# Optimization experiments

Measured on AMD Instinct MI355X. Metric: run time of the kernel, lower is better.

## Reference

```python
import jax, jax.numpy as jnp
import numpy as np
from jax import lax

B, T, IN, H = 32, 512, 512, 512
NUM_LAYERS, NUM_DIR = 2, 2


def _lstm_layer(inputs, Wx, Wh, bx, bh, reverse):
    """inputs: [T,B,D]; Wx: [4H,D]; Wh: [4H,H]; bx,bh: [4H]. Returns (hs [T,B,H], hT, cT)."""
    Tn, Bn, _ = inputs.shape
    Hn = Wh.shape[1]
    # Precompute input-to-hidden projections for all timesteps (one big GEMM).
    xg = jnp.einsum('tbd,gd->tbg', inputs, Wx) + bx + bh  # [T,B,4H]
    if reverse:
        xg = xg[::-1]

    def step(carry, xg_t):
        h, c = carry
        g = xg_t + h @ Wh.T  # [B,4H]
        i, f, gg, o = jnp.split(g, 4, axis=-1)  # PyTorch LSTM gate order i,f,g,o
        i = jax.nn.sigmoid(i)
        f = jax.nn.sigmoid(f)
        gg = jnp.tanh(gg)
        o = jax.nn.sigmoid(o)
        c = f * c + i * gg
        h = o * jnp.tanh(c)
        return (h, c), h

    h0 = jnp.zeros((Bn, Hn), dtype=inputs.dtype)
    (hT, cT), hs = lax.scan(step, (h0, h0), xg)
    if reverse:
        hs = hs[::-1]
    return hs, hT, cT


def setup_inputs() -> dict:
    key = jax.random.key(0)
    ks = jax.random.split(key, 20)
    std = 1.0 / np.sqrt(H)
    u = lambda k, shp: jax.random.uniform(k, shp, jnp.float32, -std, std)
    inp = {
        'x': jax.random.normal(ks[0], (B, T, IN), jnp.float32),
        # layer 0: input dim IN, stacked over 2 directions
        'Wx_l0': u(ks[1], (NUM_DIR, 4 * H, IN)),
        'Wh_l0': u(ks[2], (NUM_DIR, 4 * H, H)),
        'bx_l0': u(ks[3], (NUM_DIR, 4 * H)),
        'bh_l0': u(ks[4], (NUM_DIR, 4 * H)),
        # layer 1: input dim 2H (bidirectional concat)
        'Wx_l1': u(ks[5], (NUM_DIR, 4 * H, NUM_DIR * H)),
        'Wh_l1': u(ks[6], (NUM_DIR, 4 * H, H)),
        'bx_l1': u(ks[7], (NUM_DIR, 4 * H)),
        'bh_l1': u(ks[8], (NUM_DIR, 4 * H)),
    }
    return inp


def reference(x, Wx_l0, Wh_l0, bx_l0, bh_l0, Wx_l1, Wh_l1, bx_l1, bh_l1):
    layer_params = [(Wx_l0, Wh_l0, bx_l0, bh_l0), (Wx_l1, Wh_l1, bx_l1, bh_l1)]
    inputs = jnp.transpose(x, (1, 0, 2))  # [T,B,IN] (batch_first -> time-major)
    h_list, c_list = [], []
    for layer in range(NUM_LAYERS):
        Wx, Wh, bx, bh = layer_params[layer]
        dir_outs = []
        for d in range(NUM_DIR):
            hs, hT, cT = _lstm_layer(inputs, Wx[d], Wh[d], bx[d], bh[d], reverse=(d == 1))
            dir_outs.append(hs)
            h_list.append(hT)
            c_list.append(cT)
        inputs = jnp.concatenate(dir_outs, axis=-1)  # [T,B,2H] (dropout=0.0)
    output = jnp.transpose(inputs, (1, 0, 2))  # [B,T,2H]
    h_n = jnp.stack(h_list)  # [num_layers*num_dir, B, H]
    c_n = jnp.stack(c_list)
    return output, h_n, c_n
```

## Files before the change

### kernel.cpp

```cpp
#include <hip/hip_runtime.h>

typedef _Float16 f16;
typedef _Float16 f16x2 __attribute__((ext_vector_type(2)));
typedef _Float16 f16x4 __attribute__((ext_vector_type(4)));
typedef _Float16 f16x8 __attribute__((ext_vector_type(8)));
typedef float f32x4 __attribute__((ext_vector_type(4)));

#define AS1 __attribute__((address_space(1)))
#define AS3 __attribute__((address_space(3)))

static __device__ __forceinline__ float sigf(float x) { return 1.f / (1.f + __expf(-x)); }
static __device__ __forceinline__ float tanh_f(float x) { return 2.f / (1.f + __expf(-2.f * x)) - 1.f; }

__global__ void f2h_kernel(const float* __restrict__ in, f16* __restrict__ out, int n4) {
  const int i = blockIdx.x * blockDim.x + threadIdx.x;
  if (i >= n4) return;
  const float4 v = ((const float4*)in)[i];
  f16x4 o;
  o[0] = (f16)v.x; o[1] = (f16)v.y; o[2] = (f16)v.z; o[3] = (f16)v.w;
  ((f16x4*)out)[i] = o;
}

__global__ void bias_kernel(const float* __restrict__ a, const float* __restrict__ b,
                            float* __restrict__ o, int n) {
  const int i = blockIdx.x * blockDim.x + threadIdx.x;
  if (i < n) o[i] = a[i] + b[i];
}

__global__ __launch_bounds__(256) void gemm_xg(const f16* __restrict__ A,
                                               const f16* __restrict__ Bt,
                                               const float* __restrict__ bias,
                                               f16* __restrict__ outp, int K) {
  __shared__ f16 As[128 * 64];
  __shared__ f16 Bs[128 * 64];
  const int tid = threadIdx.x;
  const int w = tid >> 6, l = tid & 63;
  const int m0 = blockIdx.x << 7, n0 = blockIdx.y << 7;
  const int wm = w >> 1, wn = w & 1;
  f32x4 acc[4][4] = {};

  const int lr8 = l >> 3, lc8 = l & 7;
  const int gcol = (lc8 ^ lr8) << 3;

  for (int k0 = 0; k0 < K; k0 += 64) {
    __syncthreads();
#pragma unroll
    for (int j = 0; j < 4; ++j) {
      const int i = (w << 2) + j;
      const f16* ga = A + (size_t)(m0 + (i << 3) + lr8) * K + (k0 + gcol);
      __builtin_amdgcn_global_load_lds((const AS1 void*)ga, (AS3 void*)(As + (i << 9)), 16, 0, 0);
      const f16* gb = Bt + (size_t)(n0 + (i << 3) + lr8) * K + (k0 + gcol);
      __builtin_amdgcn_global_load_lds((const AS1 void*)gb, (AS3 void*)(Bs + (i << 9)), 16, 0, 0);
    }
    asm volatile("s_waitcnt vmcnt(0)" ::: "memory");
    __syncthreads();

#pragma unroll
    for (int kk = 0; kk < 2; ++kk) {
      const int cb = (kk << 6) + ((l >> 4) << 4);
      f16x8 af[4], bf[4];
#pragma unroll
      for (int a = 0; a < 4; ++a) {
        const int r = (wm << 6) + (a << 4) + (l & 15);
        af[a] = *(const f16x8*)((const char*)As + r * 128 + (cb ^ ((r & 7) << 4)));
      }
#pragma unroll
      for (int b = 0; b < 4; ++b) {
        const int r = (wn << 6) + (b << 4) + (l & 15);
        bf[b] = *(const f16x8*)((const char*)Bs + r * 128 + (cb ^ ((r & 7) << 4)));
      }
#pragma unroll
      for (int a = 0; a < 4; ++a)
#pragma unroll
        for (int b = 0; b < 4; ++b)
          acc[a][b] = __builtin_amdgcn_mfma_f32_16x16x32_f16(af[a], bf[b], acc[a][b], 0, 0, 0);
    }
  }

#pragma unroll
  for (int b = 0; b < 4; ++b) {
    const int col = n0 + (wn << 6) + (b << 4) + (l & 15);
    const float bv = bias[col];
    f16* ob = outp + (size_t)(col >> 11) * (16384ull * 2048) + (col & 2047);
#pragma unroll
    for (int a = 0; a < 4; ++a) {
      const int row0 = m0 + (wm << 6) + (a << 4) + ((l >> 4) << 2);
#pragma unroll
      for (int r = 0; r < 4; ++r)
        ob[(size_t)(row0 + r) * 2048] = (f16)(acc[a][b][r] + bv);
    }
  }
}

__global__ __launch_bounds__(256) void lstm_scan(const f16* __restrict__ Whb,
                                                 const f16* __restrict__ xg,
                                                 unsigned long long* __restrict__ ring,
                                                 f16* __restrict__ h0_all,
                                                 float* __restrict__ outf,
                                                 float* __restrict__ hn,
                                                 float* __restrict__ cn,
                                                 const int layer) {
  __shared__ f16 Wh_s[64 * 512];
  __shared__ f16 h_s[32 * 512];
  __shared__ float G_s[4 * 32 * 18];

  const int tid = threadIdx.x;
  const int dir = blockIdx.x >> 5;
  const int s = blockIdx.x & 31;
  const int w = tid >> 6, l = tid & 63;

#pragma unroll
  for (int j = 0; j < 16; ++j) {
    const int chunk = (j << 8) + tid;
    const int lr = chunk >> 6;
    const int cbyte = (chunk & 63) << 4;
    const int g = lr >> 4, u = lr & 15;
    const char* src = (const char*)Whb + (((size_t)dir * 2048 + (g << 9) + (s << 4) + u) << 10) + cbyte;
    const uint4 v = *(const uint4*)src;
    *(uint4*)((char*)Wh_s + (lr << 10) + (cbyte ^ ((lr & 7) << 4))) = v;
  }

  unsigned long long* rdir = ring + ((size_t)dir << 15);
  const int bb = tid >> 3;
  const int up = tid & 7;

  float c0 = 0.f, c1 = 0.f;
  __syncthreads();

#pragma unroll 1
  for (int t = 0; t < 512; ++t) {
    const int tau = dir ? (511 - t) : t;
    const f16* xr = xg + (((size_t)dir * 16384 + (size_t)bb * 512 + (size_t)tau) << 11) + (s << 4) + (up << 1);
    const f16x2 xv0 = *(const f16x2*)(xr);
    const f16x2 xv1 = *(const f16x2*)(xr + 512);
    const f16x2 xv2 = *(const f16x2*)(xr + 1024);
    const f16x2 xv3 = *(const f16x2*)(xr + 1536);

    float pi0 = 0.f, pi1 = 0.f, pf0 = 0.f, pf1 = 0.f, pg0 = 0.f, pg1 = 0.f, po0 = 0.f, po1 = 0.f;

    if (t > 0) {
      const unsigned tgt = (unsigned)t;
      const unsigned long long* rs = rdir + ((size_t)(t & 3) << 13);
      unsigned long long v[8][4];
#pragma unroll
      for (int j = 0; j < 8; ++j) {
        const int chunk = (j << 8) + tid;
        const unsigned long long* sp = rs + ((chunk >> 6) << 8) + ((chunk & 63) << 2);
#pragma unroll
        for (int q = 0; q < 4; ++q)
          v[j][q] = __hip_atomic_load(sp + q, __ATOMIC_RELAXED, __HIP_MEMORY_SCOPE_AGENT);
      }
      {
        const unsigned long long* sp = rs + ((tid >> 6) << 8) + ((tid & 63) << 2);
        int guard = 0;
        while (!(((unsigned)v[0][0] == tgt) & ((unsigned)v[0][1] == tgt) &
                 ((unsigned)v[0][2] == tgt) & ((unsigned)v[0][3] == tgt))) {
#pragma unroll
          for (int q = 0; q < 4; ++q)
            v[0][q] = __hip_atomic_load(sp + q, __ATOMIC_RELAXED, __HIP_MEMORY_SCOPE_AGENT);
          if (++guard > (1 << 20)) break;
        }
      }
      {
        bool ok[8];
        ok[0] = true;
        int remaining = 0;
#pragma unroll
        for (int j = 1; j < 8; ++j) {
          ok[j] = (((unsigned)v[j][0] == tgt) & ((unsigned)v[j][1] == tgt) &
                   ((unsigned)v[j][2] == tgt) & ((unsigned)v[j][3] == tgt));
          remaining += ok[j] ? 0 : 1;
        }
        int guard = 0;
        while (remaining && ++guard <= (1 << 20)) {
#pragma unroll
          for (int j = 1; j < 8; ++j) {
            if (!ok[j]) {
              const int chunk = (j << 8) + tid;
              const unsigned long long* sp = rs + ((chunk >> 6) << 8) + ((chunk & 63) << 2);
#pragma unroll
              for (int q = 0; q < 4; ++q)
                v[j][q] = __hip_atomic_load(sp + q, __ATOMIC_RELAXED, __HIP_MEMORY_SCOPE_AGENT);
            }
          }
#pragma unroll
          for (int j = 1; j < 8; ++j) {
            if (!ok[j]) {
              if (((unsigned)v[j][0] == tgt) & ((unsigned)v[j][1] == tgt) &
                  ((unsigned)v[j][2] == tgt) & ((unsigned)v[j][3] == tgt)) {
                ok[j] = true;
                --remaining;
              }
            }
          }
        }
      }
#pragma unroll
      for (int j = 0; j < 8; ++j) {
        const int chunk = (j << 8) + tid;
        const int b = chunk >> 6;
        uint4 d;
        d.x = (unsigned)(v[j][0] >> 32);
        d.y = (unsigned)(v[j][1] >> 32);
        d.z = (unsigned)(v[j][2] >> 32);
        d.w = (unsigned)(v[j][3] >> 32);
        const int cbyte = (chunk & 63) << 4;
        *(uint4*)((char*)h_s + (b << 10) + (cbyte ^ ((b & 7) << 4))) = d;
      }
      __syncthreads();

      f32x4 acc0 = {}, acc1 = {};
#pragma unroll
      for (int kk = 0; kk < 16; ++kk) {
        const int cb = (kk << 6) + ((l >> 4) << 4);
        const int ra0 = l & 15;
        const int ra1 = 16 + ra0;
        const int rb = (w << 4) + ra0;
        const f16x8 a0 = *(const f16x8*)((const char*)h_s + (ra0 << 10) + (cb ^ ((ra0 & 7) << 4)));
        const f16x8 a1 = *(const f16x8*)((const char*)h_s + (ra1 << 10) + (cb ^ ((ra1 & 7) << 4)));
        const f16x8 bv = *(const f16x8*)((const char*)Wh_s + (rb << 10) + (cb ^ ((rb & 7) << 4)));
        acc0 = __builtin_amdgcn_mfma_f32_16x16x32_f16(a0, bv, acc0, 0, 0, 0);
        acc1 = __builtin_amdgcn_mfma_f32_16x16x32_f16(a1, bv, acc1, 0, 0, 0);
      }
#pragma unroll
      for (int r = 0; r < 4; ++r) {
        const int dr = ((l >> 4) << 2) + r;
        G_s[((w << 5) + dr) * 18 + (l & 15)] = acc0[r];
        G_s[((w << 5) + 16 + dr) * 18 + (l & 15)] = acc1[r];
      }
      __syncthreads();

      const float* gp = G_s + bb * 18 + (up << 1);
      const float2 vi = *(const float2*)(gp);
      const float2 vf = *(const float2*)(gp + 576);
      const float2 vg = *(const float2*)(gp + 1152);
      const float2 vo = *(const float2*)(gp + 1728);
      pi0 = vi.x; pi1 = vi.y; pf0 = vf.x; pf1 = vf.y;
      pg0 = vg.x; pg1 = vg.y; po0 = vo.x; po1 = vo.y;
    }

    pi0 += (float)xv0[0]; pi1 += (float)xv0[1];
    pf0 += (float)xv1[0]; pf1 += (float)xv1[1];
    pg0 += (float)xv2[0]; pg1 += (float)xv2[1];
    po0 += (float)xv3[0]; po1 += (float)xv3[1];

    const float i0 = sigf(pi0), i1 = sigf(pi1);
    const float f0 = sigf(pf0), f1 = sigf(pf1);
    const float g0 = tanh_f(pg0), g1 = tanh_f(pg1);
    const float o0 = sigf(po0), o1 = sigf(po1);
    c0 = f0 * c0 + i0 * g0;
    c1 = f1 * c1 + i1 * g1;
    const float h0v = o0 * tanh_f(c0);
    const float h1v = o1 * tanh_f(c1);

    union { f16x2 h2; unsigned u; } pk;
    pk.h2[0] = (f16)h0v; pk.h2[1] = (f16)h1v;

    {
      const size_t ridx = ((size_t)((t + 1) & 3) << 13) + ((size_t)bb << 8) + (s << 3) + up;
      const unsigned long long pv = ((unsigned long long)pk.u << 32) | (unsigned long long)(t + 1);
      __hip_atomic_store(rdir + ridx, pv, __ATOMIC_RELAXED, __HIP_MEMORY_SCOPE_AGENT);
    }

    const size_t orow = (((size_t)bb * 512 + (size_t)tau) << 10) + ((size_t)dir << 9) + (s << 4) + (up << 1);
    if (layer == 0) {
      *(unsigned*)(h0_all + orow) = pk.u;
    } else {
      *(float2*)(outf + orow) = make_float2(h0v, h1v);
    }
    if (t == 511) {
      const size_t nidx = (((size_t)(layer << 1) + (size_t)dir) << 14) + ((size_t)bb << 9) + (s << 4) + (up << 1);
      *(float2*)(hn + nidx) = make_float2(h0v, h1v);
      *(float2*)(cn + nidx) = make_float2(c0, c1);
    }
  }
}

extern "C" void kernel_launch(void* const* d_in, const int* in_sizes, int n_in,
                              void* d_out, int out_size, void* d_ws, size_t ws_size,
                              hipStream_t stream) {
  const float* x = (const float*)d_in[0];
  const float* Wx0 = (const float*)d_in[1];
  const float* Wh0 = (const float*)d_in[2];
  const float* bx0 = (const float*)d_in[3];
  const float* bh0 = (const float*)d_in[4];
  const float* Wx1 = (const float*)d_in[5];
  const float* Wh1 = (const float*)d_in[6];
  const float* bx1 = (const float*)d_in[7];
  const float* bh1 = (const float*)d_in[8];

  char* ws = (char*)d_ws;
  size_t off = 0;
  auto alloc = [&](size_t b) { char* p = ws + off; off += (b + 255) & ~(size_t)255; return p; };
  f16* xg = (f16*)alloc(2ull * 16384 * 2048 * 2);
  f16* x_h = (f16*)alloc(16384ull * 512 * 2);
  f16* h0a = (f16*)alloc(16384ull * 1024 * 2);
  f16* Wx0h = (f16*)alloc(2ull * 2048 * 512 * 2);
  f16* Wh0h = (f16*)alloc(2ull * 2048 * 512 * 2);
  f16* Wx1h = (f16*)alloc(2ull * 2048 * 1024 * 2);
  f16* Wh1h = (f16*)alloc(2ull * 2048 * 512 * 2);
  float* bias0 = (float*)alloc(4096 * 4);
  float* bias1 = (float*)alloc(4096 * 4);
  const size_t RB = 2ull * 4 * 32 * 256 * 8;
  unsigned long long* ring0 = (unsigned long long*)alloc(RB);
  unsigned long long* ring1 = (unsigned long long*)alloc(RB);
  if (off > ws_size) return;

  float* outp = (float*)d_out;
  float* hn = outp + 16384ull * 1024;
  float* cn = hn + 4ull * 32 * 512;

  hipMemsetAsync(ring0, 0, 2 * RB, stream);

  f2h_kernel<<<dim3(2097152 / 256), 256, 0, stream>>>(x, x_h, 2097152);
  f2h_kernel<<<dim3(524288 / 256), 256, 0, stream>>>(Wx0, Wx0h, 524288);
  f2h_kernel<<<dim3(524288 / 256), 256, 0, stream>>>(Wh0, Wh0h, 524288);
  f2h_kernel<<<dim3(1048576 / 256), 256, 0, stream>>>(Wx1, Wx1h, 1048576);
  f2h_kernel<<<dim3(524288 / 256), 256, 0, stream>>>(Wh1, Wh1h, 524288);
  bias_kernel<<<16, 256, 0, stream>>>(bx0, bh0, bias0, 4096);
  bias_kernel<<<16, 256, 0, stream>>>(bx1, bh1, bias1, 4096);

  dim3 g(128, 32);
  gemm_xg<<<g, 256, 0, stream>>>(x_h, Wx0h, bias0, xg, 512);
  lstm_scan<<<64, 256, 0, stream>>>(Wh0h, xg, ring0, h0a, nullptr, hn, cn, 0);
  gemm_xg<<<g, 256, 0, stream>>>(h0a, Wx1h, bias1, xg, 1024);
  lstm_scan<<<64, 256, 0, stream>>>(Wh1h, xg, ring1, nullptr, outp, hn, cn, 1);
}
```

Baseline: 5.140 ms.

## Split batch into two half-groups and prefetch next group's hidden state

The recurrent step now processes the 32-row batch as two 16-row groups, each waiting only on its half of the ring buffer, computing one MFMA tile, and publishing its h. While one group computes, the ring loads for the other group (or the next timestep) are issued ahead, so cross-block polling latency overlaps with compute. The first timestep is peeled so it skips the GEMM. The cost is two extra barriers per timestep, and half the threads sit idle in each group's gate phase.

```diff
diff --git a/kernel.cpp b/kernel.cpp
--- a/kernel.cpp
+++ b/kernel.cpp
@@ -101,7 +101,7 @@
                                                  float* __restrict__ cn,
                                                  const int layer) {
   __shared__ f16 Wh_s[64 * 512];
-  __shared__ f16 h_s[32 * 512];
+  __shared__ f16 h_s[16 * 512];
   __shared__ float G_s[4 * 32 * 18];
 
   const int tid = threadIdx.x;
@@ -123,155 +123,193 @@
   unsigned long long* rdir = ring + ((size_t)dir << 15);
   const int bb = tid >> 3;
   const int up = tid & 7;
+  const int myg = bb >> 4;
 
   float c0 = 0.f, c1 = 0.f;
   __syncthreads();
 
-#pragma unroll 1
-  for (int t = 0; t < 512; ++t) {
-    const int tau = dir ? (511 - t) : t;
-    const f16* xr = xg + (((size_t)dir * 16384 + (size_t)bb * 512 + (size_t)tau) << 11) + (s << 4) + (up << 1);
+  {
+    const int tau0 = dir ? 511 : 0;
+    const f16* xr = xg + (((size_t)dir * 16384 + (size_t)bb * 512 + tau0) << 11) + (s << 4) + (up << 1);
     const f16x2 xv0 = *(const f16x2*)(xr);
     const f16x2 xv1 = *(const f16x2*)(xr + 512);
     const f16x2 xv2 = *(const f16x2*)(xr + 1024);
     const f16x2 xv3 = *(const f16x2*)(xr + 1536);
-
-    float pi0 = 0.f, pi1 = 0.f, pf0 = 0.f, pf1 = 0.f, pg0 = 0.f, pg1 = 0.f, po0 = 0.f, po1 = 0.f;
-
-    if (t > 0) {
+    const float i0 = sigf((float)xv0[0]), i1 = sigf((float)xv0[1]);
+    const float f0 = sigf((float)xv1[0]), f1 = sigf((float)xv1[1]);
+    const float g0 = tanh_f((float)xv2[0]), g1 = tanh_f((float)xv2[1]);
+    const float o0 = sigf((float)xv3[0]), o1 = sigf((float)xv3[1]);
+    c0 = i0 * g0;
+    c1 = i1 * g1;
+    const float h0v = o0 * tanh_f(c0);
+    const float h1v = o1 * tanh_f(c1);
+    union { f16x2 h2; unsigned u; } pk;
+    pk.h2[0] = (f16)h0v; pk.h2[1] = (f16)h1v;
+    const size_t ridx = ((size_t)1 << 13) + ((size_t)bb << 8) + (s << 3) + up;
+    const unsigned long long pv = ((unsigned long long)pk.u << 32) | 1ull;
+    __hip_atomic_store(rdir + ridx, pv, __ATOMIC_RELAXED, __HIP_MEMORY_SCOPE_AGENT);
+    const size_t orow = (((size_t)bb * 512 + (size_t)tau0) << 10) + ((size_t)dir << 9) + (s << 4) + (up << 1);
+    if (layer == 0) *(unsigned*)(h0_all + orow) = pk.u;
+    else            *(float2*)(outf + orow) = make_float2(h0v, h1v);
+  }
+
+  unsigned long long sv[4][4];
+  {
+    const unsigned long long* nb = rdir + ((size_t)1 << 13);
+#pragma unroll
+    for (int j = 0; j < 4; ++j) {
+      const unsigned long long* sp = nb + (((j << 8) + tid) << 2);
+#pragma unroll
+      for (int q = 0; q < 4; ++q)
+        sv[j][q] = __hip_atomic_load(sp + q, __ATOMIC_RELAXED, __HIP_MEMORY_SCOPE_AGENT);
+    }
+  }
+
+#pragma unroll 1
+  for (int t = 1; t < 512; ++t) {
+    const int tau = dir ? (511 - t) : t;
+#pragma unroll
+    for (int gp = 0; gp < 2; ++gp) {
       const unsigned tgt = (unsigned)t;
-      const unsigned long long* rs = rdir + ((size_t)(t & 3) << 13);
-      unsigned long long v[8][4];
-#pragma unroll
-      for (int j = 0; j < 8; ++j) {
-        const int chunk = (j << 8) + tid;
-        const unsigned long long* sp = rs + ((chunk >> 6) << 8) + ((chunk & 63) << 2);
-#pragma unroll
-        for (int q = 0; q < 4; ++q)
-          v[j][q] = __hip_atomic_load(sp + q, __ATOMIC_RELAXED, __HIP_MEMORY_SCOPE_AGENT);
-      }
+      const unsigned long long* gb = rdir + ((size_t)(t & 3) << 13) + (gp << 12);
+
       {
-        const unsigned long long* sp = rs + ((tid >> 6) << 8) + ((tid & 63) << 2);
+        const unsigned long long* sp = gb + (tid << 2);
         int guard = 0;
-        while (!(((unsigned)v[0][0] == tgt) & ((unsigned)v[0][1] == tgt) &
-                 ((unsigned)v[0][2] == tgt) & ((unsigned)v[0][3] == tgt))) {
+        while (!(((unsigned)sv[0][0] == tgt) & ((unsigned)sv[0][1] == tgt) &
+                 ((unsigned)sv[0][2] == tgt) & ((unsigned)sv[0][3] == tgt))) {
 #pragma unroll
           for (int q = 0; q < 4; ++q)
-            v[0][q] = __hip_atomic_load(sp + q, __ATOMIC_RELAXED, __HIP_MEMORY_SCOPE_AGENT);
+            sv[0][q] = __hip_atomic_load(sp + q, __ATOMIC_RELAXED, __HIP_MEMORY_SCOPE_AGENT);
           if (++guard > (1 << 20)) break;
         }
       }
       {
-        bool ok[8];
-        ok[0] = true;
-        int remaining = 0;
-#pragma unroll
-        for (int j = 1; j < 8; ++j) {
-          ok[j] = (((unsigned)v[j][0] == tgt) & ((unsigned)v[j][1] == tgt) &
-                   ((unsigned)v[j][2] == tgt) & ((unsigned)v[j][3] == tgt));
-          remaining += ok[j] ? 0 : 1;
+        bool ok1 = (((unsigned)sv[1][0] == tgt) & ((unsigned)sv[1][1] == tgt) &
+                    ((unsigned)sv[1][2] == tgt) & ((unsigned)sv[1][3] == tgt));
+        bool ok2 = (((unsigned)sv[2][0] == tgt) & ((unsigned)sv[2][1] == tgt) &
+                    ((unsigned)sv[2][2] == tgt) & ((unsigned)sv[2][3] == tgt));
+        bool ok3 = (((unsigned)sv[3][0] == tgt) & ((unsigned)sv[3][1] == tgt) &
+                    ((unsigned)sv[3][2] == tgt) & ((unsigned)sv[3][3] == tgt));
+        int guard = 0;
+        while ((!ok1 || !ok2 || !ok3) && ++guard <= (1 << 20)) {
+          if (!ok1) {
+            const unsigned long long* sp = gb + (((1 << 8) + tid) << 2);
+#pragma unroll
+            for (int q = 0; q < 4; ++q)
+              sv[1][q] = __hip_atomic_load(sp + q, __ATOMIC_RELAXED, __HIP_MEMORY_SCOPE_AGENT);
+          }
+          if (!ok2) {
+            const unsigned long long* sp = gb + (((2 << 8) + tid) << 2);
+#pragma unroll
+            for (int q = 0; q < 4; ++q)
+              sv[2][q] = __hip_atomic_load(sp + q, __ATOMIC_RELAXED, __HIP_MEMORY_SCOPE_AGENT);
+          }
+          if (!ok3) {
+            const unsigned long long* sp = gb + (((3 << 8) + tid) << 2);
+#pragma unroll
+            for (int q = 0; q < 4; ++q)
+              sv[3][q] = __hip_atomic_load(sp + q, __ATOMIC_RELAXED, __HIP_MEMORY_SCOPE_AGENT);
+          }
+          ok1 = (((unsigned)sv[1][0] == tgt) & ((unsigned)sv[1][1] == tgt) &
+                 ((unsigned)sv[1][2] == tgt) & ((unsigned)sv[1][3] == tgt));
+          ok2 = (((unsigned)sv[2][0] == tgt) & ((unsigned)sv[2][1] == tgt) &
+                 ((unsigned)sv[2][2] == tgt) & ((unsigned)sv[2][3] == tgt));
+          ok3 = (((unsigned)sv[3][0] == tgt) & ((unsigned)sv[3][1] == tgt) &
+                 ((unsigned)sv[3][2] == tgt) & ((unsigned)sv[3][3] == tgt));
         }
-        int guard = 0;
-        while (remaining && ++guard <= (1 << 20)) {
-#pragma unroll
-          for (int j = 1; j < 8; ++j) {
-            if (!ok[j]) {
-              const int chunk = (j << 8) + tid;
-              const unsigned long long* sp = rs + ((chunk >> 6) << 8) + ((chunk & 63) << 2);
-#pragma unroll
-              for (int q = 0; q < 4; ++q)
-                v[j][q] = __hip_atomic_load(sp + q, __ATOMIC_RELAXED, __HIP_MEMORY_SCOPE_AGENT);
-            }
-          }
-#pragma unroll
-          for (int j = 1; j < 8; ++j) {
-            if (!ok[j]) {
-              if (((unsigned)v[j][0] == tgt) & ((unsigned)v[j][1] == tgt) &
-                  ((unsigned)v[j][2] == tgt) & ((unsigned)v[j][3] == tgt)) {
-                ok[j] = true;
-                --remaining;
-              }
-            }
-          }
+      }
+#pragma unroll
+      for (int j = 0; j < 4; ++j) {
+        const int idx = (j << 8) + tid;
+        const int r = idx >> 6;
+        uint4 d;
+        d.x = (unsigned)(sv[j][0] >> 32);
+        d.y = (unsigned)(sv[j][1] >> 32);
+        d.z = (unsigned)(sv[j][2] >> 32);
+        d.w = (unsigned)(sv[j][3] >> 32);
+        const int cbyte = (idx & 63) << 4;
+        *(uint4*)((char*)h_s + (r << 10) + (cbyte ^ ((r & 7) << 4))) = d;
+      }
+
+      const bool act = (myg == gp);
+      f16x2 xv0 = {}, xv1 = {}, xv2 = {}, xv3 = {};
+      if (act) {
+        const f16* xr = xg + (((size_t)dir * 16384 + (size_t)bb * 512 + (size_t)tau) << 11) + (s << 4) + (up << 1);
+        xv0 = *(const f16x2*)(xr);
+        xv1 = *(const f16x2*)(xr + 512);
+        xv2 = *(const f16x2*)(xr + 1024);
+        xv3 = *(const f16x2*)(xr + 1536);
+      }
+
+      {
+        const int ot = gp ? (t + 1) : t;
+        const unsigned long long* nb = rdir + ((size_t)(ot & 3) << 13) + ((gp ^ 1) << 12);
+#pragma unroll
+        for (int j = 0; j < 4; ++j) {
+          const unsigned long long* sp = nb + (((j << 8) + tid) << 2);
+#pragma unroll
+          for (int q = 0; q < 4; ++q)
+            sv[j][q] = __hip_atomic_load(sp + q, __ATOMIC_RELAXED, __HIP_MEMORY_SCOPE_AGENT);
         }
       }
-#pragma unroll
-      for (int j = 0; j < 8; ++j) {
-        const int chunk = (j << 8) + tid;
-        const int b = chunk >> 6;
-        uint4 d;
-        d.x = (unsigned)(v[j][0] >> 32);
-        d.y = (unsigned)(v[j][1] >> 32);
-        d.z = (unsigned)(v[j][2] >> 32);
-        d.w = (unsigned)(v[j][3] >> 32);
-        const int cbyte = (chunk & 63) << 4;
-        *(uint4*)((char*)h_s + (b << 10) + (cbyte ^ ((b & 7) << 4))) = d;
-      }
+
       __syncthreads();
 
-      f32x4 acc0 = {}, acc1 = {};
+      f32x4 acc0 = {};
 #pragma unroll
       for (int kk = 0; kk < 16; ++kk) {
         const int cb = (kk << 6) + ((l >> 4) << 4);
         const int ra0 = l & 15;
-        const int ra1 = 16 + ra0;
         const int rb = (w << 4) + ra0;
         const f16x8 a0 = *(const f16x8*)((const char*)h_s + (ra0 << 10) + (cb ^ ((ra0 & 7) << 4)));
-        const f16x8 a1 = *(const f16x8*)((const char*)h_s + (ra1 << 10) + (cb ^ ((ra1 & 7) << 4)));
         const f16x8 bv = *(const f16x8*)((const char*)Wh_s + (rb << 10) + (cb ^ ((rb & 7) << 4)));
         acc0 = __builtin_amdgcn_mfma_f32_16x16x32_f16(a0, bv, acc0, 0, 0, 0);
-        acc1 = __builtin_amdgcn_mfma_f32_16x16x32_f16(a1, bv, acc1, 0, 0, 0);
       }
 #pragma unroll
       for (int r = 0; r < 4; ++r) {
         const int dr = ((l >> 4) << 2) + r;
         G_s[((w << 5) + dr) * 18 + (l & 15)] = acc0[r];
-        G_s[((w << 5) + 16 + dr) * 18 + (l & 15)] = acc1[r];
       }
       __syncthreads();
 
-      const float* gp = G_s + bb * 18 + (up << 1);
-      const float2 vi = *(const float2*)(gp);
-      const float2 vf = *(const float2*)(gp + 576);
-      const float2 vg = *(const float2*)(gp + 1152);
-      const float2 vo = *(const float2*)(gp + 1728);
-      pi0 = vi.x; pi1 = vi.y; pf0 = vf.x; pf1 = vf.y;
-      pg0 = vg.x; pg1 = vg.y; po0 = vo.x; po1 = vo.y;
-    }
-
-    pi0 += (float)xv0[0]; pi1 += (float)xv0[1];
-    pf0 += (float)xv1[0]; pf1 += (float)xv1[1];
-    pg0 += (float)xv2[0]; pg1 += (float)xv2[1];
-    po0 += (float)xv3[0]; po1 += (float)xv3[1];
-
-    const float i0 = sigf(pi0), i1 = sigf(pi1);
-    const float f0 = sigf(pf0), f1 = sigf(pf1);
-    const float g0 = tanh_f(pg0), g1 = tanh_f(pg1);
-    const float o0 = sigf(po0), o1 = sigf(po1);
-    c0 = f0 * c0 + i0 * g0;
-    c1 = f1 * c1 + i1 * g1;
-    const float h0v = o0 * tanh_f(c0);
-    const float h1v = o1 * tanh_f(c1);
-
-    union { f16x2 h2; unsigned u; } pk;
-    pk.h2[0] = (f16)h0v; pk.h2[1] = (f16)h1v;
-
-    {
-      const size_t ridx = ((size_t)((t + 1) & 3) << 13) + ((size_t)bb << 8) + (s << 3) + up;
-      const unsigned long long pv = ((unsigned long long)pk.u << 32) | (unsigned long long)(t + 1);
-      __hip_atomic_store(rdir + ridx, pv, __ATOMIC_RELAXED, __HIP_MEMORY_SCOPE_AGENT);
-    }
-
-    const size_t orow = (((size_t)bb * 512 + (size_t)tau) << 10) + ((size_t)dir << 9) + (s << 4) + (up << 1);
-    if (layer == 0) {
-      *(unsigned*)(h0_all + orow) = pk.u;
-    } else {
-      *(float2*)(outf + orow) = make_float2(h0v, h1v);
-    }
-    if (t == 511) {
-      const size_t nidx = (((size_t)(layer << 1) + (size_t)dir) << 14) + ((size_t)bb << 9) + (s << 4) + (up << 1);
-      *(float2*)(hn + nidx) = make_float2(h0v, h1v);
-      *(float2*)(cn + nidx) = make_float2(c0, c1);
+      if (act) {
+        const int rl = bb & 15;
+        const float* gpos = G_s + rl * 18 + (up << 1);
+        const float2 vi = *(const float2*)(gpos);
+        const float2 vf = *(const float2*)(gpos + 576);
+        const float2 vg = *(const float2*)(gpos + 1152);
+        const float2 vo = *(const float2*)(gpos + 1728);
+        const float pi0 = vi.x + (float)xv0[0], pi1 = vi.y + (float)xv0[1];
+        const float pf0 = vf.x + (float)xv1[0], pf1 = vf.y + (float)xv1[1];
+        const float pg0 = vg.x + (float)xv2[0], pg1 = vg.y + (float)xv2[1];
+        const float po0 = vo.x + (float)xv3[0], po1 = vo.y + (float)xv3[1];
+
+        const float i0 = sigf(pi0), i1 = sigf(pi1);
+        const float f0 = sigf(pf0), f1 = sigf(pf1);
+        const float g0 = tanh_f(pg0), g1 = tanh_f(pg1);
+        const float o0 = sigf(po0), o1 = sigf(po1);
+        c0 = f0 * c0 + i0 * g0;
+        c1 = f1 * c1 + i1 * g1;
+        const float h0v = o0 * tanh_f(c0);
+        const float h1v = o1 * tanh_f(c1);
+
+        union { f16x2 h2; unsigned u; } pk;
+        pk.h2[0] = (f16)h0v; pk.h2[1] = (f16)h1v;
+
+        const size_t ridx = ((size_t)((t + 1) & 3) << 13) + ((size_t)bb << 8) + (s << 3) + up;
+        const unsigned long long pv = ((unsigned long long)pk.u << 32) | (unsigned long long)(t + 1);
+        __hip_atomic_store(rdir + ridx, pv, __ATOMIC_RELAXED, __HIP_MEMORY_SCOPE_AGENT);
+
+        const size_t orow = (((size_t)bb * 512 + (size_t)tau) << 10) + ((size_t)dir << 9) + (s << 4) + (up << 1);
+        if (layer == 0) *(unsigned*)(h0_all + orow) = pk.u;
+        else            *(float2*)(outf + orow) = make_float2(h0v, h1v);
+        if (t == 511) {
+          const size_t nidx = (((size_t)(layer << 1) + (size_t)dir) << 14) + ((size_t)bb << 9) + (s << 4) + (up << 1);
+          *(float2*)(hn + nidx) = make_float2(h0v, h1v);
+          *(float2*)(cn + nidx) = make_float2(c0, c1);
+        }
+      }
     }
   }
 }
```

After: 7.191 ms. 1.4x slower.
